# Kernel tuning notes

Measured on AMD Instinct MI355X. Metric: run time of the kernel, lower is better.

## Reference

```python
import jax, jax.numpy as jnp
import numpy as np


def setup_inputs() -> dict:
    key = jax.random.key(0)
    ks = jax.random.split(key, 8)
    B, S, H, E = 4, 4096, 768, 64
    hidden_states = jax.random.normal(ks[0], (B, S, H), dtype=jnp.float32)
    attention_mask = jnp.ones((B, S), dtype=jnp.float32)
    entity_positions = jax.random.randint(ks[1], (B, E), 0, S)
    scale = 1.0 / np.sqrt(H)
    Wq = jax.random.normal(ks[2], (H, H), dtype=jnp.float32) * scale
    bq = jnp.zeros((H,), dtype=jnp.float32)
    Wk = jax.random.normal(ks[3], (H, H), dtype=jnp.float32) * scale
    bk = jnp.zeros((H,), dtype=jnp.float32)
    Wv = jax.random.normal(ks[4], (H, H), dtype=jnp.float32) * scale
    bv = jnp.zeros((H,), dtype=jnp.float32)
    return {"hidden_states": hidden_states, "attention_mask": attention_mask,
            "entity_positions": entity_positions,
            "Wq": Wq, "bq": bq, "Wk": Wk, "bk": bk, "Wv": Wv, "bv": bv}


def reference(hidden_states, attention_mask, entity_positions, Wq, bq, Wk, bk, Wv, bv):
    B, S, H = hidden_states.shape
    scaling = jnp.sqrt(jnp.asarray(H, dtype=jnp.float32))
    # Linear layers (torch: x @ W.T + b)
    q = jnp.einsum('bsh,oh->bso', hidden_states, Wq) + bq
    k = jnp.einsum('bsh,oh->bso', hidden_states, Wk) + bk
    v = jnp.einsum('bsh,oh->bso', hidden_states, Wv) + bv
    scores = jnp.einsum('bqh,bkh->bqk', q, k) / scaling  # [B,S,S]
    # Entity bias: +1.0 added to every row at each entity column (duplicates accumulate).
    # Equivalent to a per-key-column bias broadcast over query rows.
    bias_cols = jnp.zeros((B, S), dtype=scores.dtype)
    batch_idx = jnp.arange(B)[:, None]  # [B,1] broadcast against [B,E]
    bias_cols = bias_cols.at[batch_idx, entity_positions].add(1.0)
    scores = scores + bias_cols[:, None, :]
    # Attention mask over key columns.
    scores = scores + (1.0 - attention_mask)[:, None, :] * -10000.0
    probs = jax.nn.softmax(scores, axis=-1)
    context = jnp.einsum('bqk,bkh->bqh', probs, v)
    return context
```

## Files before the change

kernel.cpp:

```cpp
#include <hip/hip_runtime.h>


typedef short bf16x8 __attribute__((ext_vector_type(8)));
typedef float f32x4 __attribute__((ext_vector_type(4)));
typedef float f32x16 __attribute__((ext_vector_type(16)));

#define MFMA16(a, b, c) __builtin_amdgcn_mfma_f32_16x16x32_bf16(a, b, c, 0, 0, 0)
#define MFMA32(a, b, c) __builtin_amdgcn_mfma_f32_32x32x16_bf16(a, b, c, 0, 0, 0)

#define ASM_BAR() asm volatile("s_barrier" ::: "memory")
#define ASM_WAITV0() asm volatile("s_waitcnt vmcnt(0)" ::: "memory")
#define ASM_WAITV4() asm volatile("s_waitcnt vmcnt(4)" ::: "memory")
#define ASM_WAITV6() asm volatile("s_waitcnt vmcnt(6)" ::: "memory")
#define ASM_WAITL0() asm volatile("s_waitcnt lgkmcnt(0)" ::: "memory")

__device__ __forceinline__ unsigned short f2bf(float f) {
  unsigned u = __float_as_uint(f);
  u = u + 0x7FFFu + ((u >> 16) & 1u);
  return (unsigned short)(u >> 16);
}

__device__ __forceinline__ void gll16(const void* g, void* l) {
  __builtin_amdgcn_global_load_lds(
      (const __attribute__((address_space(1))) unsigned int*)g,
      (__attribute__((address_space(3))) unsigned int*)l, 16, 0, 0);
}

#define SCALE_L2E 0.05205877316f
#define LOG2E 1.4426950408889634f

#define HS_BLOCKS 12288
#define W_BLOCKS 1728
#define KB_BLOCKS 64
__global__ void prep_kernel(const float* __restrict__ hs, unsigned short* __restrict__ ohs,
                            const float* __restrict__ w0, const float* __restrict__ w1,
                            const float* __restrict__ w2, unsigned short* __restrict__ o0,
                            unsigned short* __restrict__ o1, unsigned short* __restrict__ o2,
                            const float* __restrict__ mask, const int* __restrict__ ep,
                            float* __restrict__ kb) {
  __shared__ int eps[64];
  const int bid = blockIdx.x;
  const int t = threadIdx.x;
  if (bid < HS_BLOCKS) {
    const int i = (bid * 256 + t) * 4;
    float4 v = *(const float4*)(hs + i);
    *(ushort4*)(ohs + i) = make_ushort4(f2bf(v.x), f2bf(v.y), f2bf(v.z), f2bf(v.w));
  } else if (bid < HS_BLOCKS + W_BLOCKS) {
    const int wb = bid - HS_BLOCKS;
    const int which = wb / 576;
    const float* s = which == 0 ? w0 : (which == 1 ? w1 : w2);
    unsigned short* d = which == 0 ? o0 : (which == 1 ? o1 : o2);
    const int i = ((wb - which * 576) * 256 + t) * 4;
    float4 v = *(const float4*)(s + i);
    *(ushort4*)(d + i) = make_ushort4(f2bf(v.x), f2bf(v.y), f2bf(v.z), f2bf(v.w));
  } else {
    const int s = (bid - HS_BLOCKS - W_BLOCKS) * 256 + t;
    const int b = s >> 12;
    if (t < 64) eps[t] = ep[b * 64 + t];
    __syncthreads();
    const int sp = s & 4095;
    float cnt = 0.0f;
#pragma unroll 8
    for (int e = 0; e < 64; e++) cnt += (eps[e] == sp) ? 1.0f : 0.0f;
    kb[s] = (1.0f - mask[s]) * (-10000.0f * LOG2E) + cnt * LOG2E;
  }
}

__global__ __launch_bounds__(256, 3) void gemm_qkv_kernel(
    const unsigned short* __restrict__ hsb, const unsigned short* __restrict__ Wqb,
    const unsigned short* __restrict__ Wkb, const unsigned short* __restrict__ Wvb,
    const float* __restrict__ bq, const float* __restrict__ bk, const float* __restrict__ bv,
    unsigned short* __restrict__ Qb, unsigned short* __restrict__ Kb,
    unsigned short* __restrict__ Vt) {
  __shared__ __align__(16) unsigned short Ab[3][128 * 32];
  __shared__ __align__(16) unsigned short Bb[3][128 * 32];

  const int bid = blockIdx.x;
  const int t = threadIdx.x;
  const int lane = t & 63;
  const int w = t >> 6;
  const int wm = w & 1, wn = w >> 1;

  const bool is_vt = bid >= 1536;
  const unsigned short* srcA;
  const unsigned short* srcB;
  int m0, n0, z = 0;
  if (!is_vt) {
    z = bid / 768;
    const int r = bid - z * 768;
    m0 = (r & 127) * 128;
    n0 = (r >> 7) * 128;
    srcA = hsb;
    srcB = z ? Wkb : Wqb;
  } else {
    const int r = bid - 1536;
    const int mx = r % 6;
    m0 = mx * 128;
    n0 = (r / 6) * 128;
    srcA = Wvb;
    srcB = hsb;
  }

  f32x4 acc[4][4] = {};

  auto issueT = [&](const unsigned short* src, int base, int kk, unsigned short* dst) {
#pragma unroll
    for (int r = 0; r < 2; r++) {
      int u = r * 256 + t;
      int o = u >> 2, cc = u & 3;
      int c = cc ^ ((o >> 1) & 3);
      gll16(src + (size_t)(base + o) * 768 + kk + c * 8, dst + u * 8);
    }
  };

  issueT(srcA, m0, 0, Ab[0]);
  issueT(srcB, n0, 0, Bb[0]);
  issueT(srcA, m0, 32, Ab[1]);
  issueT(srcB, n0, 32, Bb[1]);
  ASM_WAITV4();
  ASM_BAR();

  for (int k = 0; k < 24; k++) {
    const int buf = k % 3;
    if (k < 22) {
      const int nb = (k + 2) % 3;
      issueT(srcA, m0, (k + 2) * 32, Ab[nb]);
      issueT(srcB, n0, (k + 2) * 32, Bb[nb]);
    }
    bf16x8 af[4], bfr[4];
#pragma unroll
    for (int mt = 0; mt < 4; mt++) {
      int row = wm * 64 + mt * 16 + (lane & 15);
      int cc = (lane >> 4) ^ ((row >> 1) & 3);
      af[mt] = *(const bf16x8*)(&Ab[buf][row * 32 + cc * 8]);
    }
#pragma unroll
    for (int nt = 0; nt < 4; nt++) {
      int row = wn * 64 + nt * 16 + (lane & 15);
      int cc = (lane >> 4) ^ ((row >> 1) & 3);
      bfr[nt] = *(const bf16x8*)(&Bb[buf][row * 32 + cc * 8]);
    }
#pragma unroll
    for (int mt = 0; mt < 4; mt++)
#pragma unroll
      for (int nt = 0; nt < 4; nt++) acc[mt][nt] = MFMA16(af[mt], bfr[nt], acc[mt][nt]);
    if (k < 22) {
      ASM_WAITV4();
    } else {
      ASM_WAITV0();
    }
    ASM_BAR();
  }

  if (!is_vt) {
    const float* bias = z ? bk : bq;
    unsigned short* out = z ? Kb : Qb;
#pragma unroll
    for (int nt = 0; nt < 4; nt++) {
      int col = n0 + wn * 64 + nt * 16 + (lane & 15);
      float bv_ = bias[col];
#pragma unroll
      for (int mt = 0; mt < 4; mt++) {
#pragma unroll
        for (int i = 0; i < 4; i++) {
          int row = m0 + wm * 64 + mt * 16 + (lane >> 4) * 4 + i;
          out[(size_t)row * 768 + col] = f2bf(acc[mt][nt][i] + bv_);
        }
      }
    }
  } else {
#pragma unroll
    for (int mt = 0; mt < 4; mt++) {
#pragma unroll
      for (int i = 0; i < 4; i++) {
        int row_o = m0 + wm * 64 + mt * 16 + (lane >> 4) * 4 + i;
        float bb = bv[row_o];
#pragma unroll
        for (int nt = 0; nt < 4; nt++) {
          int mcol = n0 + wn * 64 + nt * 16 + (lane & 15);
          int bat = mcol >> 12, s = mcol & 4095;
          Vt[(size_t)bat * 768 * 4096 + (size_t)row_o * 4096 + s] = f2bf(acc[mt][nt][i] + bb);
        }
      }
    }
  }
}

__global__ __launch_bounds__(512, 2) void flash_kernel(const unsigned short* __restrict__ Qb,
                                                       const unsigned short* __restrict__ Kb,
                                                       const unsigned short* __restrict__ Vt,
                                                       const float* __restrict__ KB,
                                                       float* __restrict__ out) {
  __shared__ __align__(16) unsigned short kbuf[32 * 768];
  __shared__ __align__(16) unsigned short vbuf[768 * 32];
  __shared__ __align__(16) unsigned short pbuf[4 * 64 * 8];
  __shared__ __align__(16) float sx[4 * 2 * 64 * 16];
  __shared__ __align__(16) float kb_lds[4096];
  __shared__ float st_l[64];

  const int t = threadIdx.x;
  const int lane = t & 63;
  const int w = t >> 6;
  const int rg = w & 1, hg = w >> 1;
  const int mt2 = w & 1, dg = w >> 1;
  const int flat = blockIdx.x;
  const int b = flat & 3, qt = flat >> 2;
  const int q0 = qt * 64;

  const unsigned short* Qg = Qb + (size_t)b * 4096 * 768;
  const unsigned short* Kg = Kb + (size_t)b * 4096 * 768;
  const unsigned short* Vg = Vt + (size_t)b * 768 * 4096;
  const float* KBb = KB + b * 4096;

  bf16x8 qf[12];
  {
    const unsigned short* qp =
        Qg + (size_t)(q0 + rg * 32 + (lane & 31)) * 768 + hg * 192 + (lane >> 5) * 8;
#pragma unroll
    for (int c = 0; c < 12; c++) qf[c] = *(const bf16x8*)(qp + c * 16);
  }
#pragma unroll
  for (int r = 0; r < 2; r++) {
    int i = t * 8 + r * 4;
    *(float4*)(kb_lds + i) = *(const float4*)(KBb + i);
  }

  int kidx[12];
  {
    const int key = lane & 31, l5 = lane >> 5, sw = (key >> 1) & 3;
#pragma unroll
    for (int c = 0; c < 12; c++) {
      int g = hg * 24 + c * 2 + l5;
      kidx[c] = ((g >> 2) * 128 + key * 4 + ((g & 3) ^ sw)) * 8;
    }
  }
  int vbase;
  {
    int d0 = dg * 192 + (lane & 15);
    vbase = (d0 * 4 + ((lane >> 4) ^ ((d0 >> 1) & 3))) * 8;
  }
  int pidx0, pidx1;
  {
    int g2 = lane >> 4;
    int r0 = mt2 * 32 + (lane & 15);
    int r1 = r0 + 16;
    pidx0 = (g2 * 64 + (r0 ^ (g2 * 2) ^ ((r0 >> 2) & 1))) * 8;
    pidx1 = (g2 * 64 + (r1 ^ (g2 * 2) ^ ((r1 >> 2) & 1))) * 8;
  }
  const int s_rg = t >> 8, s_q = (t >> 6) & 3, s_l = t & 63;
  const int col = s_l & 31;
  const int row_b = s_rg * 32 + 8 * s_q + 4 * (s_l >> 5);
  int pslot[4];
#pragma unroll
  for (int jj = 0; jj < 4; jj++) {
    int rw = row_b + jj;
    pslot[jj] = ((col >> 3) * 64 + (rw ^ ((col >> 3) * 2) ^ ((rw >> 2) & 1))) * 8 + (col & 7);
  }
  float* sxw = sx + hg * 2048 + (rg * 64 + lane) * 16;
  const int wswz = (lane >> 1) & 3;
  const float* sxr = sx + (s_rg * 64 + s_l) * 16 + (s_q ^ ((s_l >> 1) & 3)) * 4;

  f32x4 oacc[24] = {};
  float racc0 = 0.0f, racc1 = 0.0f, racc2 = 0.0f, racc3 = 0.0f;

  auto issueK = [&](int j) {
#pragma unroll
    for (int r = 0; r < 6; r++) {
      int u = r * 512 + t;
      int ks = u >> 7, rem = u & 127, key = rem >> 2, cs = rem & 3;
      int c = cs ^ ((key >> 1) & 3);
      gll16(Kg + (size_t)(j * 32 + key) * 768 + ks * 32 + c * 8, &kbuf[u * 8]);
    }
  };
  auto issueV = [&](int j) {
#pragma unroll
    for (int r = 0; r < 6; r++) {
      int u = r * 512 + t;
      int d = u >> 2, cs = u & 3;
      int c = cs ^ ((d >> 1) & 3);
      gll16(Vg + (size_t)d * 4096 + j * 32 + c * 8, &vbuf[u * 8]);
    }
  };

  issueK(0);
  ASM_WAITV0();
  ASM_BAR();

  for (int j = 0; j < 128; j++) {
    issueV(j);
    f32x16 s = {};
#pragma unroll
    for (int c = 0; c < 12; c++) {
      bf16x8 kf = *(const bf16x8*)(kbuf + kidx[c]);
      s = MFMA32(qf[c], kf, s);
    }
#pragma unroll
    for (int i = 0; i < 4; i++) {
      *(float4*)(sxw + (i ^ wswz) * 4) =
          make_float4(s[i * 4], s[i * 4 + 1], s[i * 4 + 2], s[i * 4 + 3]);
    }
    ASM_WAITL0();
    ASM_BAR();
    if (j < 127) issueK(j + 1);
    {
      float4 a0 = *(const float4*)(sxr);
      float4 a1 = *(const float4*)(sxr + 2048);
      float4 a2 = *(const float4*)(sxr + 4096);
      float4 a3 = *(const float4*)(sxr + 6144);
      float kbias = kb_lds[j * 32 + col];
      float e0 = __builtin_amdgcn_exp2f(fmaf(a0.x + a1.x + a2.x + a3.x, SCALE_L2E, kbias));
      float e1 = __builtin_amdgcn_exp2f(fmaf(a0.y + a1.y + a2.y + a3.y, SCALE_L2E, kbias));
      float e2 = __builtin_amdgcn_exp2f(fmaf(a0.z + a1.z + a2.z + a3.z, SCALE_L2E, kbias));
      float e3 = __builtin_amdgcn_exp2f(fmaf(a0.w + a1.w + a2.w + a3.w, SCALE_L2E, kbias));
      pbuf[pslot[0]] = f2bf(e0);
      pbuf[pslot[1]] = f2bf(e1);
      pbuf[pslot[2]] = f2bf(e2);
      pbuf[pslot[3]] = f2bf(e3);
      racc0 += e0;
      racc1 += e1;
      racc2 += e2;
      racc3 += e3;
    }
    ASM_WAITL0();
    if (j < 127) {
      ASM_WAITV6();
    } else {
      ASM_WAITV0();
    }
    ASM_BAR();
    {
      bf16x8 pf0 = *(const bf16x8*)(pbuf + pidx0);
      bf16x8 pf1 = *(const bf16x8*)(pbuf + pidx1);
#pragma unroll
      for (int dt = 0; dt < 12; dt++) {
        bf16x8 vf = *(const bf16x8*)(vbuf + vbase + dt * 512);
        oacc[dt] = MFMA16(pf0, vf, oacc[dt]);
        oacc[12 + dt] = MFMA16(pf1, vf, oacc[12 + dt]);
      }
    }
    ASM_WAITV0();
    ASM_BAR();
  }
#pragma unroll
  for (int m = 1; m < 32; m <<= 1) {
    racc0 += __shfl_xor(racc0, m, 32);
    racc1 += __shfl_xor(racc1, m, 32);
    racc2 += __shfl_xor(racc2, m, 32);
    racc3 += __shfl_xor(racc3, m, 32);
  }
  if ((s_l & 31) == 0) {
    st_l[row_b] = racc0;
    st_l[row_b + 1] = racc1;
    st_l[row_b + 2] = racc2;
    st_l[row_b + 3] = racc3;
  }
  __syncthreads();
#pragma unroll
  for (int pt = 0; pt < 2; pt++) {
    int rb = mt2 * 32 + pt * 16 + (lane >> 4) * 4;
    float l0 = 1.0f / st_l[rb], l1 = 1.0f / st_l[rb + 1];
    float l2 = 1.0f / st_l[rb + 2], l3 = 1.0f / st_l[rb + 3];
#pragma unroll
    for (int dt = 0; dt < 12; dt++) {
      int d = dg * 192 + dt * 16 + (lane & 15);
      size_t base = ((size_t)(b * 4096 + q0 + rb)) * 768 + d;
      out[base] = oacc[pt * 12 + dt][0] * l0;
      out[base + 768] = oacc[pt * 12 + dt][1] * l1;
      out[base + 2 * 768] = oacc[pt * 12 + dt][2] * l2;
      out[base + 3 * 768] = oacc[pt * 12 + dt][3] * l3;
    }
  }
}

extern "C" void kernel_launch(void* const* d_in, const int* in_sizes, int n_in, void* d_out,
                              int out_size, void* d_ws, size_t ws_size, hipStream_t stream) {
  const float* hs = (const float*)d_in[0];
  const float* mask = (const float*)d_in[1];
  const int* ep = (const int*)d_in[2];
  const float* Wq = (const float*)d_in[3];
  const float* bq = (const float*)d_in[4];
  const float* Wk = (const float*)d_in[5];
  const float* bk = (const float*)d_in[6];
  const float* Wv = (const float*)d_in[7];
  const float* bv = (const float*)d_in[8];
  float* outp = (float*)d_out;

  char* ws = (char*)d_ws;
  unsigned short* Qb = (unsigned short*)(ws);
  unsigned short* Kb = (unsigned short*)(ws + 25165824);
  unsigned short* Vt = (unsigned short*)(ws + 50331648);
  unsigned short* Wqb = (unsigned short*)(ws + 75497472);
  unsigned short* Wkb = (unsigned short*)(ws + 76677120);
  unsigned short* Wvb = (unsigned short*)(ws + 77856768);
  float* KBp = (float*)(ws + 79036416);
  unsigned short* Hsb = (unsigned short*)(ws + 79101952);

  prep_kernel<<<HS_BLOCKS + W_BLOCKS + KB_BLOCKS, 256, 0, stream>>>(
      hs, Hsb, Wq, Wk, Wv, Wqb, Wkb, Wvb, mask, ep, KBp);
  gemm_qkv_kernel<<<2304, 256, 0, stream>>>(Hsb, Wqb, Wkb, Wvb, bq, bk, bv, Qb, Kb, Vt);
  flash_kernel<<<256, 512, 0, stream>>>(Qb, Kb, Vt, KBp, outp);
}
```

Measured before the change: 477.7 us.

## Load V fragments directly into registers instead of staging through LDS

```diff
diff --git a/kernel.cpp b/kernel.cpp
--- a/kernel.cpp
+++ b/kernel.cpp
@@ -11,7 +11,6 @@
 #define ASM_BAR() asm volatile("s_barrier" ::: "memory")
 #define ASM_WAITV0() asm volatile("s_waitcnt vmcnt(0)" ::: "memory")
 #define ASM_WAITV4() asm volatile("s_waitcnt vmcnt(4)" ::: "memory")
-#define ASM_WAITV6() asm volatile("s_waitcnt vmcnt(6)" ::: "memory")
 #define ASM_WAITL0() asm volatile("s_waitcnt lgkmcnt(0)" ::: "memory")
 
 __device__ __forceinline__ unsigned short f2bf(float f) {
@@ -192,7 +191,6 @@
                                                        const float* __restrict__ KB,
                                                        float* __restrict__ out) {
   __shared__ __align__(16) unsigned short kbuf[32 * 768];
-  __shared__ __align__(16) unsigned short vbuf[768 * 32];
   __shared__ __align__(16) unsigned short pbuf[4 * 64 * 8];
   __shared__ __align__(16) float sx[4 * 2 * 64 * 16];
   __shared__ __align__(16) float kb_lds[4096];
@@ -234,11 +232,8 @@
       kidx[c] = ((g >> 2) * 128 + key * 4 + ((g & 3) ^ sw)) * 8;
     }
   }
-  int vbase;
-  {
-    int d0 = dg * 192 + (lane & 15);
-    vbase = (d0 * 4 + ((lane >> 4) ^ ((d0 >> 1) & 3))) * 8;
-  }
+  const unsigned short* vptr =
+      Vg + (size_t)(dg * 192 + (lane & 15)) * 4096 + (lane >> 4) * 8;
   int pidx0, pidx1;
   {
     int g2 = lane >> 4;
@@ -272,32 +267,29 @@
       gll16(Kg + (size_t)(j * 32 + key) * 768 + ks * 32 + c * 8, &kbuf[u * 8]);
     }
   };
-  auto issueV = [&](int j) {
-#pragma unroll
-    for (int r = 0; r < 6; r++) {
-      int u = r * 512 + t;
-      int d = u >> 2, cs = u & 3;
-      int c = cs ^ ((d >> 1) & 3);
-      gll16(Vg + (size_t)d * 4096 + j * 32 + c * 8, &vbuf[u * 8]);
-    }
-  };
 
   issueK(0);
   ASM_WAITV0();
   ASM_BAR();
 
   for (int j = 0; j < 128; j++) {
-    issueV(j);
-    f32x16 s = {};
-#pragma unroll
-    for (int c = 0; c < 12; c++) {
-      bf16x8 kf = *(const bf16x8*)(kbuf + kidx[c]);
-      s = MFMA32(qf[c], kf, s);
+    bf16x8 vreg[12];
+#pragma unroll
+    for (int dt = 0; dt < 12; dt++)
+      vreg[dt] = *(const bf16x8*)(vptr + (size_t)dt * 16 * 4096 + j * 32);
+    f32x16 slo = {}, shi = {};
+#pragma unroll
+    for (int c = 0; c < 12; c += 2) {
+      bf16x8 kf0 = *(const bf16x8*)(kbuf + kidx[c]);
+      bf16x8 kf1 = *(const bf16x8*)(kbuf + kidx[c + 1]);
+      slo = MFMA32(qf[c], kf0, slo);
+      shi = MFMA32(qf[c + 1], kf1, shi);
     }
 #pragma unroll
     for (int i = 0; i < 4; i++) {
       *(float4*)(sxw + (i ^ wswz) * 4) =
-          make_float4(s[i * 4], s[i * 4 + 1], s[i * 4 + 2], s[i * 4 + 3]);
+          make_float4(slo[i * 4] + shi[i * 4], slo[i * 4 + 1] + shi[i * 4 + 1],
+                      slo[i * 4 + 2] + shi[i * 4 + 2], slo[i * 4 + 3] + shi[i * 4 + 3]);
     }
     ASM_WAITL0();
     ASM_BAR();
@@ -322,20 +314,14 @@
       racc3 += e3;
     }
     ASM_WAITL0();
-    if (j < 127) {
-      ASM_WAITV6();
-    } else {
-      ASM_WAITV0();
-    }
     ASM_BAR();
     {
       bf16x8 pf0 = *(const bf16x8*)(pbuf + pidx0);
       bf16x8 pf1 = *(const bf16x8*)(pbuf + pidx1);
 #pragma unroll
       for (int dt = 0; dt < 12; dt++) {
-        bf16x8 vf = *(const bf16x8*)(vbuf + vbase + dt * 512);
-        oacc[dt] = MFMA16(pf0, vf, oacc[dt]);
-        oacc[12 + dt] = MFMA16(pf1, vf, oacc[12 + dt]);
+        oacc[dt] = MFMA16(pf0, vreg[dt], oacc[dt]);
+        oacc[12 + dt] = MFMA16(pf1, vreg[dt], oacc[12 + dt]);
       }
     }
     ASM_WAITV0();
```

Measured after the change: 692.7 us. 45.0% more time.
